# Kernel optimization log

Hardware: AMD Instinct MI355X
Metric: run time of the kernel (lower is better)

Reference implementation:

```python
import jax, jax.numpy as jnp
import numpy as np

FRAC_BIT = 12
SCALE = float(2 ** FRAC_BIT)          # 12 fractional bits
QMIN, QMAX = -32768.0, 32767.0        # signed 16-bit two's complement range


def quant16(x):
    """Quantize to signed 16-bit fixed point with 12 fractional bits.

    Matches float_to_16bits_tensor / bit_slice semantics: the bit-serial
    crossbar MVM of the sliced operands equals an exact integer product of
    these fixed-point values, rescaled back to float.
    """
    return jnp.clip(jnp.round(x * SCALE), QMIN, QMAX) / SCALE


def setup_inputs() -> dict:
    key = jax.random.key(0)
    k1, k2 = jax.random.split(key)
    x = jax.random.normal(k1, (32, 128, 56, 56), dtype=jnp.float32)
    # kaiming-ish scale so weights are well inside the fixed-point range
    weight = jax.random.normal(k2, (256, 128, 3, 3), dtype=jnp.float32) * 0.05
    return {"x": x, "weight": weight}


def reference(x, weight):
    # The nested i/j loop in the original slides a stride-1 window over the
    # zero-padded input, performing a bit-sliced crossbar MVM per pixel.
    # That is exactly conv2d(stride=1, padding=1) on 16-bit fixed-point
    # quantized input and weight (bias row in the crossbar is zero / unused).
    qx = quant16(x)
    qw = quant16(weight)
    out = jax.lax.conv_general_dilated(
        qx, qw,
        window_strides=(1, 1),
        padding=((1, 1), (1, 1)),
        dimension_numbers=("NCHW", "OIHW", "NCHW"),
    )
    return out
```

## Files before the change

kernel.cpp:

```cpp
#include <hip/hip_runtime.h>
#include <cstdint>
#include <cstddef>


typedef __attribute__((ext_vector_type(8))) short short8;
typedef __attribute__((ext_vector_type(4))) float floatx4;

#define NIMG 32
#define CIN  128
#define HW   56
#define KOUT 256
#define HP   58
#define XPAD_ELEMS ((size_t)NIMG * HP * HP * CIN)
#define WT_OFF_BYTES (XPAD_ELEMS * 2)
#define KK 1152

__device__ __forceinline__ uint16_t quant_bf16(float v) {
    float q = rintf(v * 4096.0f);
    q = fminf(fmaxf(q, -32768.0f), 32767.0f) * (1.0f / 4096.0f);
    union { float f; uint32_t u; } cv; cv.f = q;
    uint32_t u = cv.u;
    return (uint16_t)((u + 0x7fffu + ((u >> 16) & 1u)) >> 16);
}

__device__ __forceinline__ float f4c(float4 v, int k) {
    switch (k) { case 0: return v.x; case 1: return v.y;
                 case 2: return v.z; default: return v.w; }
}

__global__ __launch_bounds__(256) void quant_pad_x(const float* __restrict__ x,
                                                   uint16_t* __restrict__ xp) {
    const int b = blockIdx.x;
    const int n = b / HP, hp = b - n * HP;
    uint16_t* row = xp + (size_t)(n * HP + hp) * HP * CIN;

    if (hp == 0 || hp == HP - 1) {
        uint4 z{0, 0, 0, 0};
        uint4* d = (uint4*)row;
        for (int t = threadIdx.x; t < HP * CIN * 2 / 16; t += 256) d[t] = z;
        return;
    }
    const int h = hp - 1;
    __shared__ __align__(16) uint16_t tile[HW * 136];
    const float* src = x + (size_t)n * CIN * HW * HW + (size_t)h * HW;
    for (int t = threadIdx.x; t < 32 * 14; t += 256) {
        int cg = t / 14, w4 = t - cg * 14;
        int c4 = cg * 4;
        float4 v0 = *(const float4*)(src + (size_t)(c4 + 0) * (HW * HW) + w4 * 4);
        float4 v1 = *(const float4*)(src + (size_t)(c4 + 1) * (HW * HW) + w4 * 4);
        float4 v2 = *(const float4*)(src + (size_t)(c4 + 2) * (HW * HW) + w4 * 4);
        float4 v3 = *(const float4*)(src + (size_t)(c4 + 3) * (HW * HW) + w4 * 4);
#pragma unroll
        for (int k = 0; k < 4; ++k) {
            int w = w4 * 4 + k;
            uint32_t lo = (uint32_t)quant_bf16(f4c(v0, k)) |
                          ((uint32_t)quant_bf16(f4c(v1, k)) << 16);
            uint32_t hi = (uint32_t)quant_bf16(f4c(v2, k)) |
                          ((uint32_t)quant_bf16(f4c(v3, k)) << 16);
            *(uint2*)&tile[w * 136 + c4] = make_uint2(lo, hi);
        }
    }
    __syncthreads();
    if (threadIdx.x < 32) {
        uint4 z{0, 0, 0, 0};
        if (threadIdx.x < 16) ((uint4*)row)[threadIdx.x] = z;
        else ((uint4*)(row + 57 * CIN))[threadIdx.x - 16] = z;
    }
    uint4* dst = (uint4*)(row + CIN);
    for (int t = threadIdx.x; t < HW * 16; t += 256) {
        int w = t >> 4, c8 = (t & 15) * 8;
        dst[t] = *(const uint4*)&tile[w * 136 + c8];
    }
}

__global__ __launch_bounds__(256) void quant_w(const float* __restrict__ w,
                                               uint16_t* __restrict__ wt) {
    int i = blockIdx.x * 256 + threadIdx.x;
    int kt = i >> 14;
    int rem = i & 16383;
    int r = rem >> 6;
    int j = rem & 63;
    int tap = kt >> 1;
    int c = ((kt & 1) << 6) + j;
    wt[i] = quant_bf16(w[(size_t)(r * CIN + c) * 9 + tap]);
}


#define GLOAD(gsrc, ldst)                                                      \
    __builtin_amdgcn_global_load_lds(                                          \
        (__attribute__((address_space(1))) void*)(void*)(gsrc),                \
        (__attribute__((address_space(3))) void*)(void*)(ldst), 16, 0, 0)

#define STAGE_A(bsel, kt) do {                                                 \
    const uint16_t* as_ = wt + (size_t)(kt) * 16384 + a00;                     \
    GLOAD(as_,         &ldsA[bsel][0][(wv * 8) * 64]);                         \
    GLOAD(as_ + 4096,  &ldsA[bsel][0][(64 + wv * 8) * 64]);                    \
    GLOAD(as_ + 8192,  &ldsA[bsel][1][(wv * 8) * 64]);                         \
    GLOAD(as_ + 12288, &ldsA[bsel][1][(64 + wv * 8) * 64]);                    \
} while (0)

#define STAGE_B(bsel, kt) do {                                                 \
    const int tap_ = (kt) >> 1;                                                \
    const size_t boff_ = (size_t)((tap_ / 3) * HP + (tap_ % 3)) * CIN          \
                       + (size_t)((kt) & 1) * 64;                              \
    GLOAD(bGp[0][0] + boff_, &ldsB[bsel][0][(wv * 8) * 64]);                   \
    GLOAD(bGp[0][1] + boff_, &ldsB[bsel][0][(64 + wv * 8) * 64]);              \
    GLOAD(bGp[1][0] + boff_, &ldsB[bsel][1][(wv * 8) * 64]);                   \
    GLOAD(bGp[1][1] + boff_, &ldsB[bsel][1][(64 + wv * 8) * 64]);              \
} while (0)

#define READ_A(bsel, q4) do {                                                  \
    _Pragma("unroll")                                                          \
    for (int f_ = 0; f_ < 4; ++f_) {                                           \
        const int r_ = (q4) * 64 + f_ * 16 + m16;                              \
        ra[f_][0] = *(const short8*)&ldsA[bsel][wm][r_ * 64 + sl0];            \
        ra[f_][1] = *(const short8*)&ldsA[bsel][wm][r_ * 64 + sl1];            \
    }                                                                          \
} while (0)

#define READ_B(dst, bsel, ch) do {                                             \
    _Pragma("unroll")                                                          \
    for (int fc_ = 0; fc_ < 2; ++fc_) {                                        \
        const int r_ = bl + (ch) * 32 + fc_ * 16 + m16;                        \
        dst[fc_][0] = *(const short8*)&ldsB[bsel][bh][r_ * 64 + sl0];          \
        dst[fc_][1] = *(const short8*)&ldsB[bsel][bh][r_ * 64 + sl1];          \
    }                                                                          \
} while (0)

#define MFMA_Q(q4, ch, B) do {                                                 \
    _Pragma("unroll")                                                          \
    for (int s_ = 0; s_ < 2; ++s_)                                             \
    _Pragma("unroll")                                                          \
    for (int f_ = 0; f_ < 4; ++f_)                                             \
    _Pragma("unroll")                                                          \
    for (int c_ = 0; c_ < 2; ++c_)                                             \
        acc[q4][f_][ch][c_] = __builtin_amdgcn_mfma_f32_16x16x32_bf16(         \
            ra[f_][s_], B[c_][s_], acc[q4][f_][ch][c_], 0, 0, 0);              \
} while (0)

#define KT_BODY(bsel) do {                                                     \
    READ_A(bsel, 0);                                                           \
    READ_B(rb0, bsel, 0);                                                      \
    READ_B(rb1, bsel, 1);                                                      \
    __builtin_amdgcn_s_setprio(1);                                             \
    MFMA_Q(0, 0, rb0);                                                         \
    MFMA_Q(0, 1, rb1);                                                         \
    __builtin_amdgcn_s_setprio(0);                                             \
    READ_A(bsel, 1);                   \
    __builtin_amdgcn_s_setprio(1);                                             \
    MFMA_Q(1, 0, rb0);                                                         \
    MFMA_Q(1, 1, rb1);                                                         \
    __builtin_amdgcn_s_setprio(0);                                             \
} while (0)

#define KT_SYNC_STAGE(bsel, ktn) do {                                          \
    __builtin_amdgcn_s_barrier();                                              \
    STAGE_A(bsel, ktn); STAGE_B(bsel, ktn);                                    \
    asm volatile("s_waitcnt vmcnt(8)" ::: "memory");                           \
    __builtin_amdgcn_s_barrier();                                              \
} while (0)

__global__ __launch_bounds__(512, 2) void conv_gemm(const uint16_t* __restrict__ xp,
                                                    const uint16_t* __restrict__ wt,
                                                    float* __restrict__ out) {
    __shared__ __align__(16) uint16_t ldsA[2][2][128 * 64];
    __shared__ __align__(16) uint16_t ldsB[2][2][128 * 64];

    const int tid  = threadIdx.x;
    const int l    = tid & 63;
    const int wv   = tid >> 6;
    const int wm   = wv >> 2;
    const int wn   = wv & 3;
    const int bh   = wn >> 1;
    const int bl   = (wn & 1) * 64;
    const int srow = l >> 3;
    const int c_data = (l & 7) ^ srow;
    const int m16  = l & 15;
    const int q    = l >> 4;
    const int r7   = m16 & 7;
    const int sl0  = ((0 + q) ^ r7) * 8;
    const int sl1  = ((4 + q) ^ r7) * 8;

    const int b = blockIdx.x;
    const int pxblk = (b & 7) * 49 + (b >> 3);

    const int a00 = (wv * 8 + srow) * 64 + c_data * 8;

    const uint16_t* bGp[2][2];
#pragma unroll
    for (int h_ = 0; h_ < 2; ++h_)
#pragma unroll
        for (int j_ = 0; j_ < 2; ++j_) {
            const int row = h_ * 128 + j_ * 64 + wv * 8 + srow;
            const int p = pxblk * 256 + row;
            const int n = p / 3136; const int rem = p - n * 3136;
            const int hh = rem / HW; const int ww = rem - hh * HW;
            bGp[h_][j_] = xp + (size_t)((n * HP + hh) * HP + ww) * CIN + c_data * 8;
        }

    floatx4 acc[2][4][2][2];
#pragma unroll
    for (int a_ = 0; a_ < 2; ++a_)
#pragma unroll
        for (int f_ = 0; f_ < 4; ++f_)
#pragma unroll
            for (int c_ = 0; c_ < 2; ++c_)
#pragma unroll
                for (int d_ = 0; d_ < 2; ++d_)
                    acc[a_][f_][c_][d_] = (floatx4){0.f, 0.f, 0.f, 0.f};

    short8 ra[4][2];
    short8 rb0[2][2];
    short8 rb1[2][2];

    STAGE_A(0, 0); STAGE_B(0, 0);
    STAGE_A(1, 1); STAGE_B(1, 1);
    asm volatile("s_waitcnt vmcnt(8)" ::: "memory");
    __builtin_amdgcn_s_barrier();

#pragma unroll 1
    for (int it = 0; it < 8; ++it) {
        const int ktE = 2 * it + 2;
        const int ktO = 2 * it + 3;
        KT_BODY(0);
        KT_SYNC_STAGE(0, ktE);
        KT_BODY(1);
        KT_SYNC_STAGE(1, ktO);
    }

    KT_BODY(0);
    __builtin_amdgcn_s_barrier();
    asm volatile("s_waitcnt vmcnt(0)" ::: "memory");
    __builtin_amdgcn_s_barrier();
    KT_BODY(1);

#pragma unroll
    for (int ch = 0; ch < 2; ++ch) {
        const int p0 = pxblk * 256 + wn * 64 + ch * 32 + m16;
        const int n = p0 / 3136; const int rem0 = p0 - n * 3136;
        float* opb = out + (size_t)(n * KOUT + wm * 128) * 3136 + rem0;
#pragma unroll
        for (int q4 = 0; q4 < 2; ++q4)
#pragma unroll
            for (int f = 0; f < 4; ++f) {
                const int kl = q4 * 64 + f * 16 + q * 4;
#pragma unroll
                for (int t = 0; t < 4; ++t) {
                    float* op = opb + (size_t)(kl + t) * 3136;
                    op[0]  = acc[q4][f][ch][0][t];
                    op[16] = acc[q4][f][ch][1][t];
                }
            }
    }
}

extern "C" void kernel_launch(void* const* d_in, const int* in_sizes, int n_in,
                              void* d_out, int out_size, void* d_ws, size_t ws_size,
                              hipStream_t stream) {
    const float* x = (const float*)d_in[0];
    const float* w = (const float*)d_in[1];
    float* out = (float*)d_out;

    uint16_t* xp  = (uint16_t*)d_ws;
    uint16_t* wtb = (uint16_t*)((char*)d_ws + WT_OFF_BYTES);

    quant_pad_x<<<NIMG * HP, 256, 0, stream>>>(x, xp);
    quant_w<<<(KOUT * KK) / 256, 256, 0, stream>>>(w, wtb);

    conv_gemm<<<dim3(392), dim3(512), 0, stream>>>(xp, wtb, out);
}
```

Baseline: 208.6 us.

## Load weights directly into registers in MFMA fragment layout and halve pixel tile

The weight quantization kernel now writes weights pre-permuted into the per-lane MFMA fragment order, so each wave loads its A operands straight from global memory into registers and the weight LDS staging is removed. The pixel tile per block shrinks from 256 to 128, doubling the grid to 784 blocks, and waves are rearranged as 4x2 with 64x64 accumulators each. The intent is to cut LDS traffic and footprint and improve occupancy and load balance. In exchange, each wave re-reads the weights from global/L2 memory, which raises that traffic, and the smaller tile lowers B reuse per block.

```diff
diff --git a/kernel.cpp b/kernel.cpp
--- a/kernel.cpp
+++ b/kernel.cpp
@@ -76,13 +76,18 @@
 __global__ __launch_bounds__(256) void quant_w(const float* __restrict__ w,
                                                uint16_t* __restrict__ wt) {
     int i = blockIdx.x * 256 + threadIdx.x;
-    int kt = i >> 14;
-    int rem = i & 16383;
-    int r = rem >> 6;
-    int j = rem & 63;
-    int tap = kt >> 1;
-    int c = ((kt & 1) << 6) + j;
-    wt[i] = quant_bf16(w[(size_t)(r * CIN + c) * 9 + tap]);
+    int e = i & 7;
+    int lane = (i >> 3) & 63;
+    int r1 = i >> 9;
+    int s = r1 & 1;
+    int f = (r1 >> 1) & 3;
+    int g = (r1 >> 3) & 3;
+    int kt = r1 >> 5;
+    int row = g * 64 + f * 16 + (lane & 15);
+    int kk = kt * 64 + s * 32 + (lane >> 4) * 8 + e;
+    int tap = kk >> 7;
+    int c = kk & 127;
+    wt[i] = quant_bf16(w[(size_t)(row * CIN + c) * 9 + tap]);
 }
 
 
@@ -91,88 +96,55 @@
         (__attribute__((address_space(1))) void*)(void*)(gsrc),                \
         (__attribute__((address_space(3))) void*)(void*)(ldst), 16, 0, 0)
 
-#define STAGE_A(bsel, kt) do {                                                 \
-    const uint16_t* as_ = wt + (size_t)(kt) * 16384 + a00;                     \
-    GLOAD(as_,         &ldsA[bsel][0][(wv * 8) * 64]);                         \
-    GLOAD(as_ + 4096,  &ldsA[bsel][0][(64 + wv * 8) * 64]);                    \
-    GLOAD(as_ + 8192,  &ldsA[bsel][1][(wv * 8) * 64]);                         \
-    GLOAD(as_ + 12288, &ldsA[bsel][1][(64 + wv * 8) * 64]);                    \
-} while (0)
-
 #define STAGE_B(bsel, kt) do {                                                 \
     const int tap_ = (kt) >> 1;                                                \
     const size_t boff_ = (size_t)((tap_ / 3) * HP + (tap_ % 3)) * CIN          \
                        + (size_t)((kt) & 1) * 64;                              \
-    GLOAD(bGp[0][0] + boff_, &ldsB[bsel][0][(wv * 8) * 64]);                   \
-    GLOAD(bGp[0][1] + boff_, &ldsB[bsel][0][(64 + wv * 8) * 64]);              \
-    GLOAD(bGp[1][0] + boff_, &ldsB[bsel][1][(wv * 8) * 64]);                   \
-    GLOAD(bGp[1][1] + boff_, &ldsB[bsel][1][(64 + wv * 8) * 64]);              \
-} while (0)
-
-#define READ_A(bsel, q4) do {                                                  \
+    GLOAD(bGp[0] + boff_, &ldsB[bsel][(wv * 8) * 64]);                         \
+    GLOAD(bGp[1] + boff_, &ldsB[bsel][(64 + wv * 8) * 64]);                    \
+} while (0)
+
+#define LOAD_A(RA, kt) do {                                                    \
+    const uint16_t* a_ = aF + (size_t)(kt) * 16384;                            \
     _Pragma("unroll")                                                          \
     for (int f_ = 0; f_ < 4; ++f_) {                                           \
-        const int r_ = (q4) * 64 + f_ * 16 + m16;                              \
-        ra[f_][0] = *(const short8*)&ldsA[bsel][wm][r_ * 64 + sl0];            \
-        ra[f_][1] = *(const short8*)&ldsA[bsel][wm][r_ * 64 + sl1];            \
+        RA[f_][0] = *(const short8*)(a_ + f_ * 1024);                          \
+        RA[f_][1] = *(const short8*)(a_ + f_ * 1024 + 512);                    \
     }                                                                          \
 } while (0)
 
-#define READ_B(dst, bsel, ch) do {                                             \
-    _Pragma("unroll")                                                          \
-    for (int fc_ = 0; fc_ < 2; ++fc_) {                                        \
-        const int r_ = bl + (ch) * 32 + fc_ * 16 + m16;                        \
-        dst[fc_][0] = *(const short8*)&ldsB[bsel][bh][r_ * 64 + sl0];          \
-        dst[fc_][1] = *(const short8*)&ldsB[bsel][bh][r_ * 64 + sl1];          \
+#define READ_B(bsel) do {                                                      \
+    _Pragma("unroll")                                                          \
+    for (int fc_ = 0; fc_ < 4; ++fc_) {                                        \
+        const int r_ = wn * 64 + fc_ * 16 + m16;                               \
+        rb[fc_][0] = *(const short8*)&ldsB[bsel][r_ * 64 + sl0];               \
+        rb[fc_][1] = *(const short8*)&ldsB[bsel][r_ * 64 + sl1];               \
     }                                                                          \
 } while (0)
 
-#define MFMA_Q(q4, ch, B) do {                                                 \
+#define MFMA_KT(RA) do {                                                       \
+    __builtin_amdgcn_s_setprio(1);                                             \
     _Pragma("unroll")                                                          \
     for (int s_ = 0; s_ < 2; ++s_)                                             \
     _Pragma("unroll")                                                          \
     for (int f_ = 0; f_ < 4; ++f_)                                             \
     _Pragma("unroll")                                                          \
-    for (int c_ = 0; c_ < 2; ++c_)                                             \
-        acc[q4][f_][ch][c_] = __builtin_amdgcn_mfma_f32_16x16x32_bf16(         \
-            ra[f_][s_], B[c_][s_], acc[q4][f_][ch][c_], 0, 0, 0);              \
-} while (0)
-
-#define KT_BODY(bsel) do {                                                     \
-    READ_A(bsel, 0);                                                           \
-    READ_B(rb0, bsel, 0);                                                      \
-    READ_B(rb1, bsel, 1);                                                      \
-    __builtin_amdgcn_s_setprio(1);                                             \
-    MFMA_Q(0, 0, rb0);                                                         \
-    MFMA_Q(0, 1, rb1);                                                         \
+    for (int c_ = 0; c_ < 4; ++c_)                                             \
+        acc[f_][c_] = __builtin_amdgcn_mfma_f32_16x16x32_bf16(                 \
+            RA[f_][s_], rb[c_][s_], acc[f_][c_], 0, 0, 0);                     \
     __builtin_amdgcn_s_setprio(0);                                             \
-    READ_A(bsel, 1);                   \
-    __builtin_amdgcn_s_setprio(1);                                             \
-    MFMA_Q(1, 0, rb0);                                                         \
-    MFMA_Q(1, 1, rb1);                                                         \
-    __builtin_amdgcn_s_setprio(0);                                             \
-} while (0)
-
-#define KT_SYNC_STAGE(bsel, ktn) do {                                          \
-    __builtin_amdgcn_s_barrier();                                              \
-    STAGE_A(bsel, ktn); STAGE_B(bsel, ktn);                                    \
-    asm volatile("s_waitcnt vmcnt(8)" ::: "memory");                           \
-    __builtin_amdgcn_s_barrier();                                              \
 } while (0)
 
 __global__ __launch_bounds__(512, 2) void conv_gemm(const uint16_t* __restrict__ xp,
                                                     const uint16_t* __restrict__ wt,
                                                     float* __restrict__ out) {
-    __shared__ __align__(16) uint16_t ldsA[2][2][128 * 64];
-    __shared__ __align__(16) uint16_t ldsB[2][2][128 * 64];
+    __shared__ __align__(16) uint16_t ldsB[2][128 * 64];
 
     const int tid  = threadIdx.x;
     const int l    = tid & 63;
     const int wv   = tid >> 6;
-    const int wm   = wv >> 2;
-    const int wn   = wv & 3;
-    const int bh   = wn >> 1;
-    const int bl   = (wn & 1) * 64;
+    const int wm   = wv >> 1;
+    const int wn   = wv & 1;
     const int srow = l >> 3;
     const int c_data = (l & 7) ^ srow;
     const int m16  = l & 15;
@@ -182,75 +154,76 @@
     const int sl1  = ((4 + q) ^ r7) * 8;
 
     const int b = blockIdx.x;
-    const int pxblk = (b & 7) * 49 + (b >> 3);
-
-    const int a00 = (wv * 8 + srow) * 64 + c_data * 8;
-
-    const uint16_t* bGp[2][2];
-#pragma unroll
-    for (int h_ = 0; h_ < 2; ++h_)
-#pragma unroll
-        for (int j_ = 0; j_ < 2; ++j_) {
-            const int row = h_ * 128 + j_ * 64 + wv * 8 + srow;
-            const int p = pxblk * 256 + row;
-            const int n = p / 3136; const int rem = p - n * 3136;
-            const int hh = rem / HW; const int ww = rem - hh * HW;
-            bGp[h_][j_] = xp + (size_t)((n * HP + hh) * HP + ww) * CIN + c_data * 8;
-        }
-
-    floatx4 acc[2][4][2][2];
-#pragma unroll
-    for (int a_ = 0; a_ < 2; ++a_)
-#pragma unroll
-        for (int f_ = 0; f_ < 4; ++f_)
-#pragma unroll
-            for (int c_ = 0; c_ < 2; ++c_)
-#pragma unroll
-                for (int d_ = 0; d_ < 2; ++d_)
-                    acc[a_][f_][c_][d_] = (floatx4){0.f, 0.f, 0.f, 0.f};
-
-    short8 ra[4][2];
-    short8 rb0[2][2];
-    short8 rb1[2][2];
-
-    STAGE_A(0, 0); STAGE_B(0, 0);
-    STAGE_A(1, 1); STAGE_B(1, 1);
-    asm volatile("s_waitcnt vmcnt(8)" ::: "memory");
+    const int pxblk = (b & 7) * 98 + (b >> 3);
+
+    const uint16_t* aF = wt + (size_t)(wm * 4 * 2) * 512 + l * 8;
+
+    const uint16_t* bGp[2];
+#pragma unroll
+    for (int j_ = 0; j_ < 2; ++j_) {
+        const int row = j_ * 64 + wv * 8 + srow;
+        const int p = pxblk * 128 + row;
+        const int n = p / 3136; const int rem = p - n * 3136;
+        const int hh = rem / HW; const int ww = rem - hh * HW;
+        bGp[j_] = xp + (size_t)((n * HP + hh) * HP + ww) * CIN + c_data * 8;
+    }
+
+    floatx4 acc[4][4];
+#pragma unroll
+    for (int f_ = 0; f_ < 4; ++f_)
+#pragma unroll
+        for (int c_ = 0; c_ < 4; ++c_)
+            acc[f_][c_] = (floatx4){0.f, 0.f, 0.f, 0.f};
+
+    short8 raE[4][2];
+    short8 raO[4][2];
+    short8 rb[4][2];
+
+    STAGE_B(0, 0);
+    STAGE_B(1, 1);
+    LOAD_A(raE, 0);
+    LOAD_A(raO, 1);
+    asm volatile("s_waitcnt vmcnt(18)" ::: "memory");
     __builtin_amdgcn_s_barrier();
 
 #pragma unroll 1
     for (int it = 0; it < 8; ++it) {
-        const int ktE = 2 * it + 2;
-        const int ktO = 2 * it + 3;
-        KT_BODY(0);
-        KT_SYNC_STAGE(0, ktE);
-        KT_BODY(1);
-        KT_SYNC_STAGE(1, ktO);
-    }
-
-    KT_BODY(0);
-    __builtin_amdgcn_s_barrier();
+        const int ktE = 2 * it;
+        READ_B(0);
+        MFMA_KT(raE);
+        LOAD_A(raE, ktE + 2);
+        __builtin_amdgcn_s_barrier();
+        STAGE_B(0, ktE + 2);
+        asm volatile("s_waitcnt vmcnt(10)" ::: "memory");
+        __builtin_amdgcn_s_barrier();
+        READ_B(1);
+        MFMA_KT(raO);
+        LOAD_A(raO, ktE + 3);
+        __builtin_amdgcn_s_barrier();
+        STAGE_B(1, ktE + 3);
+        asm volatile("s_waitcnt vmcnt(10)" ::: "memory");
+        __builtin_amdgcn_s_barrier();
+    }
+
+    READ_B(0);
+    MFMA_KT(raE);
     asm volatile("s_waitcnt vmcnt(0)" ::: "memory");
     __builtin_amdgcn_s_barrier();
-    KT_BODY(1);
-
-#pragma unroll
-    for (int ch = 0; ch < 2; ++ch) {
-        const int p0 = pxblk * 256 + wn * 64 + ch * 32 + m16;
-        const int n = p0 / 3136; const int rem0 = p0 - n * 3136;
-        float* opb = out + (size_t)(n * KOUT + wm * 128) * 3136 + rem0;
-#pragma unroll
-        for (int q4 = 0; q4 < 2; ++q4)
-#pragma unroll
-            for (int f = 0; f < 4; ++f) {
-                const int kl = q4 * 64 + f * 16 + q * 4;
-#pragma unroll
-                for (int t = 0; t < 4; ++t) {
-                    float* op = opb + (size_t)(kl + t) * 3136;
-                    op[0]  = acc[q4][f][ch][0][t];
-                    op[16] = acc[q4][f][ch][1][t];
-                }
-            }
+    READ_B(1);
+    MFMA_KT(raO);
+
+#pragma unroll
+    for (int fc = 0; fc < 4; ++fc) {
+        const int p = pxblk * 128 + wn * 64 + fc * 16 + m16;
+        const int n = p / 3136; const int rem = p - n * 3136;
+        float* opb = out + (size_t)(n * KOUT + wm * 64) * 3136 + rem;
+#pragma unroll
+        for (int f = 0; f < 4; ++f) {
+            const int kl = f * 16 + q * 4;
+#pragma unroll
+            for (int t = 0; t < 4; ++t)
+                opb[(size_t)(kl + t) * 3136] = acc[f][fc][t];
+        }
     }
 }
 
@@ -267,5 +240,5 @@
     quant_pad_x<<<NIMG * HP, 256, 0, stream>>>(x, xp);
     quant_w<<<(KOUT * KK) / 256, 256, 0, stream>>>(w, wtb);
 
-    conv_gemm<<<dim3(392), dim3(512), 0, stream>>>(xp, wtb, out);
-}
+    conv_gemm<<<dim3(784), dim3(512), 0, stream>>>(xp, wtb, out);
+}
```

Result: slower. 218.0 us (+4.5%).
